# Performance work log

Measured on AMD Instinct MI355X. Metric: run time of the kernel, lower is better.

## Reference

```python
import jax, jax.numpy as jnp
import numpy as np

B, N, E, D = 32, 4096, 8192, 128


def setup_inputs() -> dict:
    key = jax.random.key(0)
    ks = jax.random.split(key, 6)
    atom_state = jax.random.normal(ks[0], (B, N, D), dtype=jnp.float32)
    messages = jax.random.normal(ks[1], (B, E, D), dtype=jnp.float32)
    connectivity = jax.random.randint(ks[2], (B, E, 2), 0, N, dtype=jnp.int32)
    kernel = jax.random.normal(ks[3], (D, 3 * D), dtype=jnp.float32) * 0.05
    recurrent_kernel = jax.random.normal(ks[4], (D, 3 * D), dtype=jnp.float32) * 0.05
    bias = jnp.zeros((2, 3 * D), dtype=jnp.float32)
    return {"atom_state": atom_state, "messages": messages,
            "connectivity": connectivity, "kernel": kernel,
            "recurrent_kernel": recurrent_kernel, "bias": bias}


def reference(atom_state, messages, connectivity, kernel, recurrent_kernel, bias):
    b, n, d = atom_state.shape
    # --- Reduce: scatter-add messages onto target atoms ---
    tgt_idx = connectivity[:, :, 1]                       # [B,E]
    offset = (jnp.arange(b, dtype=tgt_idx.dtype) * n)[:, None]
    flat_idx = (tgt_idx + offset).reshape(-1)             # [B*E]
    flat_msgs = messages.reshape(-1, d)                   # [B*E,D]
    aggregated = jax.ops.segment_sum(flat_msgs, flat_idx, num_segments=b * n)  # [B*N,D]
    # --- GRUCell (Keras default: reset_after=True, sigmoid/tanh) ---
    h = atom_state.reshape(-1, d)                         # [B*N,D]
    matrix_x = aggregated @ kernel + bias[0]              # [B*N,3D]
    matrix_h = h @ recurrent_kernel + bias[1]             # [B*N,3D]
    x_z, x_r, x_h = jnp.split(matrix_x, 3, axis=-1)
    r_z, r_r, r_h = jnp.split(matrix_h, 3, axis=-1)
    z = jax.nn.sigmoid(x_z + r_z)
    r = jax.nn.sigmoid(x_r + r_r)
    hh = jnp.tanh(x_h + r * r_h)
    h_new = z * h + (1.0 - z) * hh
    return h_new.reshape(b, n, d)
```

## Files before the change

kernel.cpp:

```cpp
#include <hip/hip_runtime.h>
#include <hip/hip_bf16.h>
#include <stdint.h>

#define BB 32
#define NN 4096
#define EE 8192
#define DD 128
#define MM (BB * NN)
#define THREE_D (3 * DD)

typedef __bf16 bf16x8 __attribute__((ext_vector_type(8)));
typedef float  f32x4  __attribute__((ext_vector_type(4)));

#define WT_OFF   0
#define OFFC_OFF ((size_t)1 << 20)
#define CSR_OFF  ((size_t)2 << 20)

__global__ __launch_bounds__(256)
void build_tables(const float* __restrict__ w0,
                  const float* __restrict__ w1,
                  const int* __restrict__ conn,
                  __bf16* __restrict__ wt,
                  int2* __restrict__ offcnt,
                  int* __restrict__ csr) {
    if (blockIdx.x >= BB) {
        int tid = (blockIdx.x - BB) * 256 + threadIdx.x;
        int mat = tid / (THREE_D * DD);
        int rem = tid % (THREE_D * DD);
        int col = rem / DD;
        int k   = rem % DD;
        const float* src = mat ? w1 : w0;
        wt[tid] = (__bf16)src[k * THREE_D + col];
        return;
    }
    __shared__ int tgtL[EE];
    __shared__ int hist[NN];
    __shared__ int part[256];
    const int b   = blockIdx.x;
    const int tid = threadIdx.x;
    const int2* c2 = (const int2*)conn + (size_t)b * EE;

    for (int k = 0; k < EE / 256; ++k) {
        int e = k * 256 + tid;
        tgtL[e] = c2[e].y;
    }
    for (int n = tid; n < NN; n += 256) hist[n] = 0;
    __syncthreads();
    for (int k = 0; k < EE / 256; ++k)
        atomicAdd(&hist[tgtL[k * 256 + tid]], 1);
    __syncthreads();

    const int c0 = tid * 16;
    int s = 0;
    for (int i = 0; i < 16; ++i) s += hist[c0 + i];
    part[tid] = s;
    __syncthreads();
    for (int d = 1; d < 256; d <<= 1) {
        int v = (tid >= d) ? part[tid - d] : 0;
        __syncthreads();
        part[tid] += v;
        __syncthreads();
    }
    int run = part[tid] - s;
    for (int i = 0; i < 16; ++i) {
        int c = hist[c0 + i];
        offcnt[(size_t)b * NN + c0 + i] = (int2){b * EE + run, c};
        hist[c0 + i] = run;
        run += c;
    }
    __syncthreads();

    for (int k = 0; k < EE / 256; ++k) {
        int e = k * 256 + tid;
        int t = tgtL[e];
        int pos = atomicAdd(&hist[t], 1);
        csr[(size_t)b * EE + pos] = b * EE + e;
    }
}

#define TPB_GEMM 8
#define AGP 136
#define HP  132
__launch_bounds__(512, 2)
__global__ void gru_gemm_fused(const float* __restrict__ messages,
                               const int2* __restrict__ offcnt,
                               const int* __restrict__ csr,
                               const float* __restrict__ h_in,
                               const __bf16* __restrict__ wt,
                               const float* __restrict__ bias,
                               float* __restrict__ out) {
    const int tid  = threadIdx.x;
    const int wave = tid >> 6;
    const int lane = tid & 63;
    const int quad = lane >> 4;
    const int l16  = lane & 15;

    __shared__ __bf16 aT[2][16 * AGP];
    __shared__ float  hT[2][16 * HP];
    __shared__ int    idsL[128][8];
    __shared__ int    cntL[128];
    __shared__ int    baseL[128];

    bf16x8 bfrag[3][2][4];
    for (int p = 0; p < 3; ++p)
        for (int m = 0; m < 2; ++m)
            for (int ko = 0; ko < 4; ++ko)
                bfrag[p][m][ko] = *(const bf16x8*)(wt
                    + ((size_t)(m * THREE_D + p * 128 + wave * 16 + l16)) * DD
                    + ko * 32 + quad * 8);

    const int j = wave * 16 + l16;
    const float b0z = bias[j];
    const float b0r = bias[DD + j];
    const float b0h = bias[2 * DD + j];
    const float b1z = bias[THREE_D + j];
    const float b1r = bias[THREE_D + DD + j];
    const float b1h = bias[THREE_D + 2 * DD + j];

    const int tile0 = blockIdx.x * TPB_GEMM;

    if (tid < 128) {
        int2 oc = offcnt[(size_t)blockIdx.x * 128 + tid];
        baseL[tid] = oc.x;
        cntL[tid]  = oc.y;
        #pragma unroll
        for (int i = 0; i < 8; ++i)
            idsL[tid][i] = csr[(size_t)oc.x + i];
    }

    f32x4 sh;
    auto load_h = [&](int tb) {
        sh = *(const f32x4*)(h_in + (size_t)tb * 2048 + tid * 4);
    };
    auto write_h = [&](int bf) {
        *(f32x4*)&hT[bf][(tid >> 5) * HP + (tid & 31) * 4] = sh;
    };

    const int ar = tid >> 4;
    const int ac = (tid & 15) * 8;
    int cnt = 0;
    int ids2[4];
    f32x4 ma[4], mb[4];
    auto msg_issue = [&](int rb) {
        if (tid < 256) {
            cnt = cntL[rb];
            int i0 = idsL[rb][0], i1 = idsL[rb][1];
            int i2 = idsL[rb][2], i3 = idsL[rb][3];
            ids2[0] = idsL[rb][4]; ids2[1] = idsL[rb][5];
            ids2[2] = idsL[rb][6]; ids2[3] = idsL[rb][7];
            int e0 = (0 < cnt) ? i0 : 0;
            int e1 = (1 < cnt) ? i1 : 0;
            int e2 = (2 < cnt) ? i2 : 0;
            int e3 = (3 < cnt) ? i3 : 0;
            ma[0] = *(const f32x4*)(messages + (size_t)e0 * DD + ac);
            mb[0] = *(const f32x4*)(messages + (size_t)e0 * DD + ac + 4);
            ma[1] = *(const f32x4*)(messages + (size_t)e1 * DD + ac);
            mb[1] = *(const f32x4*)(messages + (size_t)e1 * DD + ac + 4);
            ma[2] = *(const f32x4*)(messages + (size_t)e2 * DD + ac);
            mb[2] = *(const f32x4*)(messages + (size_t)e2 * DD + ac + 4);
            ma[3] = *(const f32x4*)(messages + (size_t)e3 * DD + ac);
            mb[3] = *(const f32x4*)(messages + (size_t)e3 * DD + ac + 4);
        }
    };
    auto agg_finish = [&](int rb, int bf) {
        if (tid < 256) {
            f32x4 s0 = (f32x4){0.f, 0.f, 0.f, 0.f};
            f32x4 s1 = (f32x4){0.f, 0.f, 0.f, 0.f};
            #pragma unroll
            for (int i = 0; i < 4; ++i)
                if (i < cnt) { s0 += ma[i]; s1 += mb[i]; }
            if (cnt > 4) {
                #pragma unroll
                for (int i = 4; i < 8; ++i) {
                    int e = (i < cnt) ? ids2[i - 4] : 0;
                    f32x4 va = *(const f32x4*)(messages + (size_t)e * DD + ac);
                    f32x4 vb = *(const f32x4*)(messages + (size_t)e * DD + ac + 4);
                    if (i < cnt) { s0 += va; s1 += vb; }
                }
                for (int i = 8; i < cnt; ++i) {
                    int e = csr[(size_t)baseL[rb] + i];
                    s0 += *(const f32x4*)(messages + (size_t)e * DD + ac);
                    s1 += *(const f32x4*)(messages + (size_t)e * DD + ac + 4);
                }
            }
            bf16x8 o;
            #pragma unroll
            for (int q = 0; q < 4; ++q) {
                o[q]     = (__bf16)s0[q];
                o[q + 4] = (__bf16)s1[q];
            }
            *(bf16x8*)&aT[bf][ar * AGP + ac] = o;
        }
    };

    __syncthreads();
    msg_issue(ar);
    load_h(tile0);
    agg_finish(ar, 0);
    write_h(0);

    int buf = 0;
    for (int t = 0; t < TPB_GEMM; ++t) {
        __syncthreads();
        const int tb = tile0 + t;
        if (t + 1 < TPB_GEMM) {
            msg_issue((t + 1) * 16 + ar);
            load_h(tb + 1);
        }

        f32x4 acc[3][2];
        for (int p = 0; p < 3; ++p)
            for (int m = 0; m < 2; ++m)
                acc[p][m] = (f32x4){0.f, 0.f, 0.f, 0.f};

        for (int ko = 0; ko < 4; ++ko) {
            bf16x8 af = *(const bf16x8*)&aT[buf][l16 * AGP + ko * 32 + quad * 8];
            f32x4 h0 = *(const f32x4*)&hT[buf][l16 * HP + ko * 32 + quad * 8];
            f32x4 h1 = *(const f32x4*)&hT[buf][l16 * HP + ko * 32 + quad * 8 + 4];
            bf16x8 hg;
            for (int i = 0; i < 4; ++i) {
                hg[i]     = (__bf16)h0[i];
                hg[i + 4] = (__bf16)h1[i];
            }
            for (int p = 0; p < 3; ++p) {
                acc[p][0] = __builtin_amdgcn_mfma_f32_16x16x32_bf16(
                    af, bfrag[p][0][ko], acc[p][0], 0, 0, 0);
                acc[p][1] = __builtin_amdgcn_mfma_f32_16x16x32_bf16(
                    hg, bfrag[p][1][ko], acc[p][1], 0, 0, 0);
            }
        }

        if (t + 1 < TPB_GEMM) agg_finish((t + 1) * 16 + ar, buf ^ 1);

        for (int rr = 0; rr < 4; ++rr) {
            int rl  = quad * 4 + rr;
            int row = tb * 16 + rl;
            float xz  = acc[0][0][rr] + b0z;
            float rz  = acc[0][1][rr] + b1z;
            float xr  = acc[1][0][rr] + b0r;
            float rrg = acc[1][1][rr] + b1r;
            float xh  = acc[2][0][rr] + b0h;
            float rh  = acc[2][1][rr] + b1h;
            float z   = 1.f / (1.f + __expf(-(xz + rz)));
            float rg  = 1.f / (1.f + __expf(-(xr + rrg)));
            float pre = xh + rg * rh;
            float hh  = 2.f / (1.f + __expf(-2.f * pre)) - 1.f;
            float hold = hT[buf][rl * HP + j];
            float o = z * hold + (1.f - z) * hh;
            out[(size_t)row * DD + j] = o;
        }

        if (t + 1 < TPB_GEMM) write_h(buf ^ 1);
        buf ^= 1;
    }
}

extern "C" void kernel_launch(void* const* d_in, const int* in_sizes, int n_in,
                              void* d_out, int out_size, void* d_ws, size_t ws_size,
                              hipStream_t stream) {
    const float* atom_state = (const float*)d_in[0];
    const float* messages   = (const float*)d_in[1];
    const int*   conn       = (const int*)d_in[2];
    const float* w0         = (const float*)d_in[3];
    const float* w1         = (const float*)d_in[4];
    const float* bias       = (const float*)d_in[5];
    float* out = (float*)d_out;

    __bf16* wt     = (__bf16*)((char*)d_ws + WT_OFF);
    int2*   offcnt = (int2*)((char*)d_ws + OFFC_OFF);
    int*    csr    = (int*)((char*)d_ws + CSR_OFF);

    build_tables<<<BB + (2 * THREE_D * DD) / 256, 256, 0, stream>>>(
        w0, w1, conn, wt, offcnt, csr);
    gru_gemm_fused<<<MM / (16 * TPB_GEMM), 512, 0, stream>>>(
        messages, offcnt, csr, atom_state, wt, bias, out);
}
```

Measured before the change: 318.7 us.

## Spread message gather over all threads and defer output stores to kernel end

The message gather now uses all 512 threads, each loading one float4 per edge, instead of only 256 threads each loading two. The h-tile stores are merged into the same finish step. Output values are kept in registers for all 8 tiles and written to global memory after the loop, so stores do not interleave with the pipelined gathers. The trade-off is 32 extra live registers per thread under a 2-blocks-per-CU launch bound, which risks spilling, and the store traffic all arrives at the end of the kernel.

```diff
diff --git a/kernel.cpp b/kernel.cpp
--- a/kernel.cpp
+++ b/kernel.cpp
@@ -10,6 +10,7 @@
 #define THREE_D (3 * DD)
 
 typedef __bf16 bf16x8 __attribute__((ext_vector_type(8)));
+typedef __bf16 bf16x4 __attribute__((ext_vector_type(4)));
 typedef float  f32x4  __attribute__((ext_vector_type(4)));
 
 #define WT_OFF   0
@@ -81,6 +82,7 @@
 #define TPB_GEMM 8
 #define AGP 136
 #define HP  132
+
 __launch_bounds__(512, 2)
 __global__ void gru_gemm_fused(const float* __restrict__ messages,
                                const int2* __restrict__ offcnt,
@@ -128,85 +130,64 @@
             idsL[tid][i] = csr[(size_t)oc.x + i];
     }
 
+    const int rb = tid >> 5;
+    const int c4 = (tid & 31) * 4;
+    int cnt = 0, base_ = 0;
+    f32x4 ma[4];
     f32x4 sh;
-    auto load_h = [&](int tb) {
-        sh = *(const f32x4*)(h_in + (size_t)tb * 2048 + tid * 4);
+
+    auto issue = [&](int t) {
+        int rbb = t * 16 + rb;
+        cnt   = cntL[rbb];
+        base_ = baseL[rbb];
+        int e0 = (0 < cnt) ? idsL[rbb][0] : 0;
+        int e1 = (1 < cnt) ? idsL[rbb][1] : 0;
+        int e2 = (2 < cnt) ? idsL[rbb][2] : 0;
+        int e3 = (3 < cnt) ? idsL[rbb][3] : 0;
+        ma[0] = *(const f32x4*)(messages + (size_t)e0 * DD + c4);
+        ma[1] = *(const f32x4*)(messages + (size_t)e1 * DD + c4);
+        ma[2] = *(const f32x4*)(messages + (size_t)e2 * DD + c4);
+        ma[3] = *(const f32x4*)(messages + (size_t)e3 * DD + c4);
+        sh = *(const f32x4*)(h_in + (size_t)(tile0 + t) * 2048 + tid * 4);
     };
-    auto write_h = [&](int bf) {
-        *(f32x4*)&hT[bf][(tid >> 5) * HP + (tid & 31) * 4] = sh;
+    auto finish = [&](int t, int bf) {
+        int rbb = t * 16 + rb;
+        f32x4 s0 = (f32x4){0.f, 0.f, 0.f, 0.f};
+        #pragma unroll
+        for (int i = 0; i < 4; ++i)
+            if (i < cnt) s0 += ma[i];
+        if (cnt > 4) {
+            #pragma unroll
+            for (int i = 4; i < 8; ++i) {
+                int e = (i < cnt) ? idsL[rbb][i] : 0;
+                f32x4 v = *(const f32x4*)(messages + (size_t)e * DD + c4);
+                if (i < cnt) s0 += v;
+            }
+            for (int i = 8; i < cnt; ++i) {
+                int e = csr[(size_t)base_ + i];
+                s0 += *(const f32x4*)(messages + (size_t)e * DD + c4);
+            }
+        }
+        bf16x4 o;
+        #pragma unroll
+        for (int q = 0; q < 4; ++q) o[q] = (__bf16)s0[q];
+        *(bf16x4*)&aT[bf][rb * AGP + c4] = o;
+        *(f32x4*)&hT[bf][rb * HP + c4] = sh;
     };
 
-    const int ar = tid >> 4;
-    const int ac = (tid & 15) * 8;
-    int cnt = 0;
-    int ids2[4];
-    f32x4 ma[4], mb[4];
-    auto msg_issue = [&](int rb) {
-        if (tid < 256) {
-            cnt = cntL[rb];
-            int i0 = idsL[rb][0], i1 = idsL[rb][1];
-            int i2 = idsL[rb][2], i3 = idsL[rb][3];
-            ids2[0] = idsL[rb][4]; ids2[1] = idsL[rb][5];
-            ids2[2] = idsL[rb][6]; ids2[3] = idsL[rb][7];
-            int e0 = (0 < cnt) ? i0 : 0;
-            int e1 = (1 < cnt) ? i1 : 0;
-            int e2 = (2 < cnt) ? i2 : 0;
-            int e3 = (3 < cnt) ? i3 : 0;
-            ma[0] = *(const f32x4*)(messages + (size_t)e0 * DD + ac);
-            mb[0] = *(const f32x4*)(messages + (size_t)e0 * DD + ac + 4);
-            ma[1] = *(const f32x4*)(messages + (size_t)e1 * DD + ac);
-            mb[1] = *(const f32x4*)(messages + (size_t)e1 * DD + ac + 4);
-            ma[2] = *(const f32x4*)(messages + (size_t)e2 * DD + ac);
-            mb[2] = *(const f32x4*)(messages + (size_t)e2 * DD + ac + 4);
-            ma[3] = *(const f32x4*)(messages + (size_t)e3 * DD + ac);
-            mb[3] = *(const f32x4*)(messages + (size_t)e3 * DD + ac + 4);
-        }
-    };
-    auto agg_finish = [&](int rb, int bf) {
-        if (tid < 256) {
-            f32x4 s0 = (f32x4){0.f, 0.f, 0.f, 0.f};
-            f32x4 s1 = (f32x4){0.f, 0.f, 0.f, 0.f};
-            #pragma unroll
-            for (int i = 0; i < 4; ++i)
-                if (i < cnt) { s0 += ma[i]; s1 += mb[i]; }
-            if (cnt > 4) {
-                #pragma unroll
-                for (int i = 4; i < 8; ++i) {
-                    int e = (i < cnt) ? ids2[i - 4] : 0;
-                    f32x4 va = *(const f32x4*)(messages + (size_t)e * DD + ac);
-                    f32x4 vb = *(const f32x4*)(messages + (size_t)e * DD + ac + 4);
-                    if (i < cnt) { s0 += va; s1 += vb; }
-                }
-                for (int i = 8; i < cnt; ++i) {
-                    int e = csr[(size_t)baseL[rb] + i];
-                    s0 += *(const f32x4*)(messages + (size_t)e * DD + ac);
-                    s1 += *(const f32x4*)(messages + (size_t)e * DD + ac + 4);
-                }
-            }
-            bf16x8 o;
-            #pragma unroll
-            for (int q = 0; q < 4; ++q) {
-                o[q]     = (__bf16)s0[q];
-                o[q + 4] = (__bf16)s1[q];
-            }
-            *(bf16x8*)&aT[bf][ar * AGP + ac] = o;
-        }
-    };
-
-    __syncthreads();
-    msg_issue(ar);
-    load_h(tile0);
-    agg_finish(ar, 0);
-    write_h(0);
-
-    int buf = 0;
+    __syncthreads();
+    issue(0);
+    finish(0, 0);
+
+    float obuf[TPB_GEMM][4];
+    int cur = 0;
+    #pragma unroll
     for (int t = 0; t < TPB_GEMM; ++t) {
         __syncthreads();
-        const int tb = tile0 + t;
-        if (t + 1 < TPB_GEMM) {
-            msg_issue((t + 1) * 16 + ar);
-            load_h(tb + 1);
-        }
+        if (t + 1 < TPB_GEMM) issue(t + 1);
+
+        const __bf16* aTc = aT[cur];
+        const float*  hTc = hT[cur];
 
         f32x4 acc[3][2];
         for (int p = 0; p < 3; ++p)
@@ -214,9 +195,9 @@
                 acc[p][m] = (f32x4){0.f, 0.f, 0.f, 0.f};
 
         for (int ko = 0; ko < 4; ++ko) {
-            bf16x8 af = *(const bf16x8*)&aT[buf][l16 * AGP + ko * 32 + quad * 8];
-            f32x4 h0 = *(const f32x4*)&hT[buf][l16 * HP + ko * 32 + quad * 8];
-            f32x4 h1 = *(const f32x4*)&hT[buf][l16 * HP + ko * 32 + quad * 8 + 4];
+            bf16x8 af = *(const bf16x8*)&aTc[l16 * AGP + ko * 32 + quad * 8];
+            f32x4 h0 = *(const f32x4*)&hTc[l16 * HP + ko * 32 + quad * 8];
+            f32x4 h1 = *(const f32x4*)&hTc[l16 * HP + ko * 32 + quad * 8 + 4];
             bf16x8 hg;
             for (int i = 0; i < 4; ++i) {
                 hg[i]     = (__bf16)h0[i];
@@ -230,11 +211,11 @@
             }
         }
 
-        if (t + 1 < TPB_GEMM) agg_finish((t + 1) * 16 + ar, buf ^ 1);
-
+        if (t + 1 < TPB_GEMM) finish(t + 1, cur ^ 1);
+
+        #pragma unroll
         for (int rr = 0; rr < 4; ++rr) {
-            int rl  = quad * 4 + rr;
-            int row = tb * 16 + rl;
+            int rl = quad * 4 + rr;
             float xz  = acc[0][0][rr] + b0z;
             float rz  = acc[0][1][rr] + b1z;
             float xr  = acc[1][0][rr] + b0r;
@@ -245,13 +226,19 @@
             float rg  = 1.f / (1.f + __expf(-(xr + rrg)));
             float pre = xh + rg * rh;
             float hh  = 2.f / (1.f + __expf(-2.f * pre)) - 1.f;
-            float hold = hT[buf][rl * HP + j];
-            float o = z * hold + (1.f - z) * hh;
-            out[(size_t)row * DD + j] = o;
-        }
-
-        if (t + 1 < TPB_GEMM) write_h(buf ^ 1);
-        buf ^= 1;
+            float hold = hTc[rl * HP + j];
+            obuf[t][rr] = z * hold + (1.f - z) * hh;
+        }
+        cur ^= 1;
+    }
+
+    #pragma unroll
+    for (int t = 0; t < TPB_GEMM; ++t) {
+        #pragma unroll
+        for (int rr = 0; rr < 4; ++rr) {
+            int row = (tile0 + t) * 16 + quad * 4 + rr;
+            out[(size_t)row * DD + j] = obuf[t][rr];
+        }
     }
 }
 
```

Result: slower. 366.4 us (+14.9%).
